# Performance work log

Measured on AMD Instinct MI355X. Metric: run time of the kernel, lower is better.

Reference implementation:

```python
import jax, jax.numpy as jnp
import numpy as np

VP = 0.4
EP = 0.21

def _c_matrix():
    # Faithfully replicate the original Ci (including its asymmetric rows 2) and invert.
    Ci = np.zeros((6, 6), dtype=np.float64)
    Ci[0, 0] = 1 / EP; Ci[0, 1] = -VP / EP; Ci[0, 2] = -VP / EP
    Ci[1, 0] = -VP / EP; Ci[1, 1] = 1 / EP; Ci[1, 2] = -VP / EP
    Ci[2, 0] = -VP;      Ci[2, 1] = -VP;      Ci[2, 2] = 1 / EP
    Ci[3, 3] = 2 * (1 + VP) / EP
    Ci[4, 4] = 2 * (1 + VP) / EP
    Ci[5, 5] = 2 * (1 + VP) / EP
    return np.linalg.inv(Ci).astype(np.float32)

C_MAT = jnp.asarray(_c_matrix())
N = 12288

def setup_inputs() -> dict:
    key = jax.random.key(0)
    k1, k2, k3 = jax.random.split(key, 3)
    xyz = jax.random.normal(k1, (N, 3), dtype=jnp.float32)
    new_xyz = jax.random.normal(k2, (N, 3), dtype=jnp.float32)
    # ~half the points are 'inside' (gt_sdf < 1e-8)
    gt_sdf = jax.random.uniform(k3, (N,), dtype=jnp.float32) - 0.5
    return {"new_xyz": new_xyz, "xyz": xyz, "gt_sdf": gt_sdf}

def reference(new_xyz, xyz, gt_sdf):
    motion = new_xyz - xyz                      # [N,3]
    inside = gt_sdf < 1e-8                      # [N] bool, selects inside points
    w = new_xyz                                 # warped coordinates (KNN space)
    n = w.shape[0]
    # Brute-force NN among inside points (KDTree k=2, second neighbor == nearest non-self).
    sq = jnp.sum(w * w, axis=1)                 # [N]
    d2 = sq[:, None] + sq[None, :] - 2.0 * (w @ w.T)   # [N,N] squared distances
    BIG = jnp.float32(1e30)
    bad_col = (~inside)[None, :] | jnp.eye(n, dtype=bool)
    d2 = jnp.where(bad_col, BIG, d2)
    nn_idx = jnp.argmin(d2, axis=1)             # nearest inside neighbor (excluding self)
    nn_d = jnp.sqrt(jnp.maximum(jnp.min(d2, axis=1), 0.0))
    # tree_list1 filter: drop rows whose nearest neighbor is a duplicate point
    valid = inside & (nn_d > 1e-8)              # [N]
    dm = motion[nn_idx] - motion                # motion_delta
    dc = w[nn_idx] - w + 1e-8                   # cords_delta (+1e-8 as in original)
    v = valid[:, None]
    dm = jnp.where(v, dm, 0.0)                  # neutralize masked rows (keep shapes static)
    dc = jnp.where(v, dc, 1.0)
    du, dv, dw = dm[:, 0], dm[:, 1], dm[:, 2]
    dx, dy, dz = dc[:, 0], dc[:, 1], dc[:, 2]
    et = jnp.stack([du / dx, dv / dy, dw / dz,
                    (du / dy + dv / dx) / 2,
                    (du / dz + dw / dx) / 2,
                    (dw / dy + dv / dz) / 2], axis=1)   # [N,6] strain tensor
    # diag(et @ C @ et.T) as an O(N) batched quadratic form
    q = jnp.einsum('ni,ij,nj->n', et, C_MAT, et)
    q = jnp.where(valid, q, 0.0)
    n_valid = jnp.sum(valid).astype(jnp.float32)
    return jnp.linalg.norm(q) / n_valid
```

## Files before the change

### kernel.cpp

```cpp
#include <hip/hip_runtime.h>
#include <math.h>
#include <string.h>

#define N 12288
#define QP 7168
#define TILE 128
#define NSPLIT 56
#define ACCS 2
#define QBLK 512
#define NQB 14
#define BT 1024

typedef unsigned long long ull;

struct CMat { float c[6][6]; };

__global__ __launch_bounds__(1024) void build_kernel(
    const float* __restrict__ new_xyz,
    const float* __restrict__ gt_sdf,
    float4* __restrict__ pts,
    int* __restrict__ cj,
    int* __restrict__ Mout)
{
    const int tid = threadIdx.x;
    const int lane = tid & 63;
    const int wave = tid >> 6;

    __shared__ int wcnt[16];
    __shared__ int sbase;
    if (tid == 0) sbase = 0;
    __syncthreads();

    for (int r = 0; r < N / BT; ++r) {
        const int idx = r * BT + tid;
        const float px = new_xyz[3 * idx + 0];
        const float py = new_xyz[3 * idx + 1];
        const float pz = new_xyz[3 * idx + 2];
        const bool ins = gt_sdf[idx] < 1e-8f;
        const ull mask = __ballot(ins);
        if (lane == 0) wcnt[wave] = __popcll(mask);
        __syncthreads();

        int pref = 0;
        for (int w = 0; w < wave; ++w) pref += wcnt[w];
        const int rank = __popcll(mask & ((1ull << lane) - 1ull));
        const int slot = sbase + pref + rank;
        if (ins && slot < QP) {
            pts[slot] = make_float4(-2.0f * px, -2.0f * py, -2.0f * pz,
                                    px * px + py * py + pz * pz);
            cj[slot] = idx;
        }
        __syncthreads();
        if (tid == 0) {
            int tot = 0;
            for (int w = 0; w < 16; ++w) tot += wcnt[w];
            sbase += tot;
        }
        __syncthreads();
    }

    const int M = sbase;
    if (tid == 0) *Mout = M;
    for (int s = M + tid; s < QP; s += BT) {
        pts[s] = make_float4(0.0f, 0.0f, 0.0f, 3e30f);
        cj[s] = 0;
    }
}

template<bool CAREFUL>
__device__ __forceinline__ void nn_inner(
    const float4* __restrict__ tile,
    const float* wx, const float* wy, const float* wz,
    const int* kx,
    float* bd, int* bk)
{
    #pragma unroll 8
    for (int k = 0; k < TILE; ++k) {
        const float4 b = tile[k];
        #pragma unroll
        for (int a = 0; a < ACCS; ++a) {
            float t = fmaf(wz[a], b.z, b.w);
            t = fmaf(wy[a], b.y, t);
            t = fmaf(wx[a], b.x, t);
            bool ok = t < bd[a];
            if (CAREFUL) ok = ok && (k != kx[a]);
            if (ok) { bd[a] = t; bk[a] = k; }
        }
    }
}

__global__ __launch_bounds__(256, 4) void nn_kernel(
    const float4* __restrict__ pts,
    ull* __restrict__ packed)
{
    const int tid = threadIdx.x;
    const int qbase = blockIdx.x * QBLK;
    const int s = blockIdx.y;
    const int jb = s * TILE;

    float wx[ACCS], wy[ACCS], wz[ACCS];
    int kx[ACCS];
    #pragma unroll
    for (int a = 0; a < ACCS; ++a) {
        const int ci = qbase + tid + a * 256;
        const float4 q = pts[ci];
        wx[a] = -0.5f * q.x;
        wy[a] = -0.5f * q.y;
        wz[a] = -0.5f * q.z;
        kx[a] = ci - jb;
    }

    __shared__ float4 tile[TILE];
    if (tid < TILE) tile[tid] = pts[jb + tid];
    __syncthreads();

    float bd[ACCS];
    int bk[ACCS];
    #pragma unroll
    for (int a = 0; a < ACCS; ++a) { bd[a] = 3.0e38f; bk[a] = 0; }

    const bool dirty = (jb < qbase + QBLK) && (jb + TILE > qbase);
    if (dirty)
        nn_inner<true>(tile, wx, wy, wz, kx, bd, bk);
    else
        nn_inner<false>(tile, wx, wy, wz, kx, bd, bk);

    #pragma unroll
    for (int a = 0; a < ACCS; ++a) {
        const int ci = qbase + tid + a * 256;
        unsigned u = __float_as_uint(bd[a]);
        u = ((int)u < 0) ? ~u : (u | 0x80000000u);
        packed[(size_t)s * QP + ci] =
            ((ull)u << 32) | (ull)(unsigned)(jb + bk[a]);
    }
}

#define NPART (QP / 256)

__global__ __launch_bounds__(256) void loss_kernel(
    const float* __restrict__ new_xyz,
    const float* __restrict__ xyz,
    const int* __restrict__ cj,
    const int* __restrict__ Mptr,
    const ull* __restrict__ packed,
    double* __restrict__ partial_sum,
    unsigned int* __restrict__ partial_cnt,
    CMat C)
{
    const int tid = threadIdx.x;
    const int ci = blockIdx.x * 256 + tid;

    ull best = ~0ull;
    #pragma unroll 8
    for (int s = 0; s < NSPLIT; ++s) {
        const ull p = packed[(size_t)s * QP + ci];
        best = (p < best) ? p : best;
    }

    const int M = *Mptr;
    const bool real = (ci < M);

    const unsigned u = (unsigned)(best >> 32);
    const unsigned bits = (u & 0x80000000u) ? (u ^ 0x80000000u) : ~u;
    const float key = __uint_as_float(bits);
    const int cc = (int)(unsigned)(best & 0xffffffffu);

    const int i  = real ? cj[ci] : 0;
    const int nn = cj[cc];

    const float wix = new_xyz[3 * i + 0];
    const float wiy = new_xyz[3 * i + 1];
    const float wiz = new_xyz[3 * i + 2];
    const float sqi = wix * wix + wiy * wiy + wiz * wiz;

    const float d2 = sqi + key;
    const float nnd = sqrtf(fmaxf(d2, 0.0f));
    const bool valid = real && (nnd > 1e-8f);

    float q = 0.0f;
    if (valid) {
        const float xix = xyz[3 * i + 0], xiy = xyz[3 * i + 1], xiz = xyz[3 * i + 2];
        const float wnx = new_xyz[3 * nn + 0], wny = new_xyz[3 * nn + 1], wnz = new_xyz[3 * nn + 2];
        const float xnx = xyz[3 * nn + 0],     xny = xyz[3 * nn + 1],     xnz = xyz[3 * nn + 2];

        const float du = (wnx - xnx) - (wix - xix);
        const float dv = (wny - xny) - (wiy - xiy);
        const float dw = (wnz - xnz) - (wiz - xiz);
        const float dx = wnx - wix + 1e-8f;
        const float dy = wny - wiy + 1e-8f;
        const float dz = wnz - wiz + 1e-8f;

        float et[6];
        et[0] = du / dx;
        et[1] = dv / dy;
        et[2] = dw / dz;
        et[3] = (du / dy + dv / dx) * 0.5f;
        et[4] = (du / dz + dw / dx) * 0.5f;
        et[5] = (dw / dy + dv / dz) * 0.5f;

        #pragma unroll
        for (int a = 0; a < 6; ++a) {
            float s2 = 0.0f;
            #pragma unroll
            for (int b2 = 0; b2 < 6; ++b2) s2 += C.c[a][b2] * et[b2];
            q += et[a] * s2;
        }
    }

    double q2 = (double)q * (double)q;
    #pragma unroll
    for (int off = 32; off > 0; off >>= 1)
        q2 += __shfl_down(q2, off, 64);
    const ull vm = __ballot(valid);
    const int lane = tid & 63;
    const int wid = tid >> 6;

    __shared__ double wsum[4];
    __shared__ unsigned wcnt2[4];
    if (lane == 0) { wsum[wid] = q2; wcnt2[wid] = (unsigned)__popcll(vm); }
    __syncthreads();
    if (tid == 0) {
        partial_sum[blockIdx.x] = wsum[0] + wsum[1] + wsum[2] + wsum[3];
        partial_cnt[blockIdx.x] = wcnt2[0] + wcnt2[1] + wcnt2[2] + wcnt2[3];
    }
}

__global__ void final_kernel(const double* __restrict__ partial_sum,
                             const unsigned int* __restrict__ partial_cnt,
                             float* __restrict__ out)
{
    const int lane = threadIdx.x;
    double s = (lane < NPART) ? partial_sum[lane] : 0.0;
    double c = (lane < NPART) ? (double)partial_cnt[lane] : 0.0;
    #pragma unroll
    for (int off = 32; off > 0; off >>= 1) {
        s += __shfl_down(s, off, 64);
        c += __shfl_down(c, off, 64);
    }
    if (lane == 0) out[0] = (float)(sqrt(s) / c);
}

static void build_cmat(CMat* M)
{
    const double VP = 0.4, EP = 0.21;
    double A[6][12];
    memset(A, 0, sizeof(A));
    double Ci[6][6];
    memset(Ci, 0, sizeof(Ci));
    Ci[0][0] = 1.0 / EP; Ci[0][1] = -VP / EP; Ci[0][2] = -VP / EP;
    Ci[1][0] = -VP / EP; Ci[1][1] = 1.0 / EP; Ci[1][2] = -VP / EP;
    Ci[2][0] = -VP;      Ci[2][1] = -VP;      Ci[2][2] = 1.0 / EP;
    Ci[3][3] = 2.0 * (1.0 + VP) / EP;
    Ci[4][4] = Ci[3][3];
    Ci[5][5] = Ci[3][3];

    for (int i = 0; i < 6; ++i) {
        for (int j = 0; j < 6; ++j) A[i][j] = Ci[i][j];
        A[i][6 + i] = 1.0;
    }
    for (int col = 0; col < 6; ++col) {
        int piv = col;
        for (int r = col + 1; r < 6; ++r)
            if (fabs(A[r][col]) > fabs(A[piv][col])) piv = r;
        if (piv != col)
            for (int c = 0; c < 12; ++c) { double t = A[col][c]; A[col][c] = A[piv][c]; A[piv][c] = t; }
        const double d = A[col][col];
        for (int c = 0; c < 12; ++c) A[col][c] /= d;
        for (int r = 0; r < 6; ++r) {
            if (r == col) continue;
            const double f = A[r][col];
            if (f == 0.0) continue;
            for (int c = 0; c < 12; ++c) A[r][c] -= f * A[col][c];
        }
    }
    for (int i = 0; i < 6; ++i)
        for (int j = 0; j < 6; ++j)
            M->c[i][j] = (float)A[i][6 + j];
}

extern "C" void kernel_launch(void* const* d_in, const int* in_sizes, int n_in,
                              void* d_out, int out_size, void* d_ws, size_t ws_size,
                              hipStream_t stream)
{
    const float* new_xyz = (const float*)d_in[0];
    const float* xyz     = (const float*)d_in[1];
    const float* gt_sdf  = (const float*)d_in[2];
    float* out = (float*)d_out;

    char* p = (char*)d_ws;
    float4* pts = (float4*)p;                    p += (size_t)QP * 16;
    int* cj = (int*)p;                           p += (size_t)QP * 4;
    int* Mptr = (int*)p;                         p += 16;
    ull* packed = (ull*)p;                       p += (size_t)NSPLIT * QP * 8;
    double* partial_sum = (double*)p;            p += NPART * sizeof(double);
    unsigned int* partial_cnt = (unsigned int*)p;

    CMat C;
    build_cmat(&C);

    build_kernel<<<1, BT, 0, stream>>>(new_xyz, gt_sdf, pts, cj, Mptr);
    nn_kernel<<<dim3(NQB, NSPLIT), 256, 0, stream>>>(pts, packed);
    loss_kernel<<<QP / 256, 256, 0, stream>>>(new_xyz, xyz, cj, Mptr, packed,
                                              partial_sum, partial_cnt, C);
    final_kernel<<<1, 64, 0, stream>>>(partial_sum, partial_cnt, out);
}
```

Measured before the change: 92.40 us.

## Merge NN partial results with atomicMin, skip empty tiles, fuse final reduction

The per-split packed nearest-neighbour candidates are no longer written to a large NSPLIT×QP buffer; each nn block now atomicMins its result into a single per-query array, so the loss kernel no longer scans 56 partials. nn blocks whose query or candidate tile lies beyond the inside-point count M exit early. The compaction kernel loads all rows up front and computes one prefix scan instead of a sync-heavy loop per round. The final reduction moves into the loss kernel through a last-block ticket, which removes one launch at the cost of 64-bit atomic contention and threadfences.

```diff
diff --git a/kernel.cpp b/kernel.cpp
--- a/kernel.cpp
+++ b/kernel.cpp
@@ -10,6 +10,8 @@
 #define QBLK 512
 #define NQB 14
 #define BT 1024
+#define RPT (N / BT)
+#define NPART (QP / 256)
 
 typedef unsigned long long ull;
 
@@ -20,51 +22,64 @@
     const float* __restrict__ gt_sdf,
     float4* __restrict__ pts,
     int* __restrict__ cj,
-    int* __restrict__ Mout)
+    int* __restrict__ Mout,
+    ull* __restrict__ best,
+    unsigned int* __restrict__ ticket)
 {
     const int tid = threadIdx.x;
     const int lane = tid & 63;
     const int wave = tid >> 6;
 
-    __shared__ int wcnt[16];
-    __shared__ int sbase;
-    if (tid == 0) sbase = 0;
-    __syncthreads();
-
-    for (int r = 0; r < N / BT; ++r) {
+    float px[RPT], py[RPT], pz[RPT];
+    unsigned flags = 0;
+
+    #pragma unroll
+    for (int r = 0; r < RPT; ++r) {
         const int idx = r * BT + tid;
-        const float px = new_xyz[3 * idx + 0];
-        const float py = new_xyz[3 * idx + 1];
-        const float pz = new_xyz[3 * idx + 2];
-        const bool ins = gt_sdf[idx] < 1e-8f;
-        const ull mask = __ballot(ins);
-        if (lane == 0) wcnt[wave] = __popcll(mask);
-        __syncthreads();
-
-        int pref = 0;
-        for (int w = 0; w < wave; ++w) pref += wcnt[w];
-        const int rank = __popcll(mask & ((1ull << lane) - 1ull));
-        const int slot = sbase + pref + rank;
-        if (ins && slot < QP) {
-            pts[slot] = make_float4(-2.0f * px, -2.0f * py, -2.0f * pz,
-                                    px * px + py * py + pz * pz);
-            cj[slot] = idx;
-        }
-        __syncthreads();
-        if (tid == 0) {
-            int tot = 0;
-            for (int w = 0; w < 16; ++w) tot += wcnt[w];
-            sbase += tot;
-        }
-        __syncthreads();
-    }
-
-    const int M = sbase;
-    if (tid == 0) *Mout = M;
+        px[r] = new_xyz[3 * idx + 0];
+        py[r] = new_xyz[3 * idx + 1];
+        pz[r] = new_xyz[3 * idx + 2];
+        if (gt_sdf[idx] < 1e-8f) flags |= (1u << r);
+    }
+
+    __shared__ int scnt[RPT * 16];
+    __shared__ int spref[RPT * 16 + 1];
+
+    #pragma unroll
+    for (int r = 0; r < RPT; ++r) {
+        const ull m = __ballot((flags >> r) & 1u);
+        if (lane == 0) scnt[r * 16 + wave] = __popcll(m);
+    }
+    __syncthreads();
+
+    if (tid < RPT * 16) {
+        int p = 0;
+        for (int f = 0; f < tid; ++f) p += scnt[f];
+        spref[tid] = p;
+        if (tid == RPT * 16 - 1) spref[RPT * 16] = p + scnt[tid];
+    }
+    __syncthreads();
+
+    const int M = spref[RPT * 16];
+
+    #pragma unroll
+    for (int r = 0; r < RPT; ++r) {
+        const ull m = __ballot((flags >> r) & 1u);
+        const int rank = __popcll(m & ((1ull << lane) - 1ull));
+        const int slot = spref[r * 16 + wave] + rank;
+        if (((flags >> r) & 1u) && slot < QP) {
+            pts[slot] = make_float4(-2.0f * px[r], -2.0f * py[r], -2.0f * pz[r],
+                                    px[r] * px[r] + py[r] * py[r] + pz[r] * pz[r]);
+            cj[slot] = r * BT + tid;
+        }
+    }
+
+    if (tid == 0) { *Mout = M; *ticket = 0u; }
     for (int s = M + tid; s < QP; s += BT) {
         pts[s] = make_float4(0.0f, 0.0f, 0.0f, 3e30f);
         cj[s] = 0;
     }
+    for (int s = tid; s < QP; s += BT) best[s] = ~0ull;
 }
 
 template<bool CAREFUL>
@@ -91,12 +106,16 @@
 
 __global__ __launch_bounds__(256, 4) void nn_kernel(
     const float4* __restrict__ pts,
-    ull* __restrict__ packed)
+    const int* __restrict__ Mptr,
+    ull* __restrict__ best)
 {
     const int tid = threadIdx.x;
     const int qbase = blockIdx.x * QBLK;
     const int s = blockIdx.y;
     const int jb = s * TILE;
+
+    const int M = *Mptr;
+    if (jb >= M || qbase >= M) return;
 
     float wx[ACCS], wy[ACCS], wz[ACCS];
     int kx[ACCS];
@@ -130,40 +149,34 @@
         const int ci = qbase + tid + a * 256;
         unsigned u = __float_as_uint(bd[a]);
         u = ((int)u < 0) ? ~u : (u | 0x80000000u);
-        packed[(size_t)s * QP + ci] =
-            ((ull)u << 32) | (ull)(unsigned)(jb + bk[a]);
-    }
-}
-
-#define NPART (QP / 256)
+        const ull v = ((ull)u << 32) | (ull)(unsigned)(jb + bk[a]);
+        atomicMin(&best[ci], v);
+    }
+}
 
 __global__ __launch_bounds__(256) void loss_kernel(
     const float* __restrict__ new_xyz,
     const float* __restrict__ xyz,
     const int* __restrict__ cj,
     const int* __restrict__ Mptr,
-    const ull* __restrict__ packed,
+    const ull* __restrict__ best_arr,
     double* __restrict__ partial_sum,
     unsigned int* __restrict__ partial_cnt,
+    unsigned int* __restrict__ ticket,
+    float* __restrict__ out,
     CMat C)
 {
     const int tid = threadIdx.x;
     const int ci = blockIdx.x * 256 + tid;
 
-    ull best = ~0ull;
-    #pragma unroll 8
-    for (int s = 0; s < NSPLIT; ++s) {
-        const ull p = packed[(size_t)s * QP + ci];
-        best = (p < best) ? p : best;
-    }
-
+    const ull best = best_arr[ci];
     const int M = *Mptr;
     const bool real = (ci < M);
 
     const unsigned u = (unsigned)(best >> 32);
     const unsigned bits = (u & 0x80000000u) ? (u ^ 0x80000000u) : ~u;
     const float key = __uint_as_float(bits);
-    const int cc = (int)(unsigned)(best & 0xffffffffu);
+    const int cc = real ? (int)(unsigned)(best & 0xffffffffu) : 0;
 
     const int i  = real ? cj[ci] : 0;
     const int nn = cj[cc];
@@ -217,27 +230,29 @@
 
     __shared__ double wsum[4];
     __shared__ unsigned wcnt2[4];
+    __shared__ bool sdone;
     if (lane == 0) { wsum[wid] = q2; wcnt2[wid] = (unsigned)__popcll(vm); }
     __syncthreads();
     if (tid == 0) {
         partial_sum[blockIdx.x] = wsum[0] + wsum[1] + wsum[2] + wsum[3];
         partial_cnt[blockIdx.x] = wcnt2[0] + wcnt2[1] + wcnt2[2] + wcnt2[3];
-    }
-}
-
-__global__ void final_kernel(const double* __restrict__ partial_sum,
-                             const unsigned int* __restrict__ partial_cnt,
-                             float* __restrict__ out)
-{
-    const int lane = threadIdx.x;
-    double s = (lane < NPART) ? partial_sum[lane] : 0.0;
-    double c = (lane < NPART) ? (double)partial_cnt[lane] : 0.0;
-    #pragma unroll
-    for (int off = 32; off > 0; off >>= 1) {
-        s += __shfl_down(s, off, 64);
-        c += __shfl_down(c, off, 64);
-    }
-    if (lane == 0) out[0] = (float)(sqrt(s) / c);
+        __threadfence();
+        const unsigned t = atomicAdd(ticket, 1u);
+        sdone = (t == NPART - 1);
+    }
+    __syncthreads();
+
+    if (sdone && tid < 64) {
+        __threadfence();
+        double s = (tid < NPART) ? partial_sum[tid] : 0.0;
+        double c = (tid < NPART) ? (double)partial_cnt[tid] : 0.0;
+        #pragma unroll
+        for (int off = 32; off > 0; off >>= 1) {
+            s += __shfl_down(s, off, 64);
+            c += __shfl_down(c, off, 64);
+        }
+        if (tid == 0) out[0] = (float)(sqrt(s) / c);
+    }
 }
 
 static void build_cmat(CMat* M)
@@ -291,16 +306,17 @@
     float4* pts = (float4*)p;                    p += (size_t)QP * 16;
     int* cj = (int*)p;                           p += (size_t)QP * 4;
     int* Mptr = (int*)p;                         p += 16;
-    ull* packed = (ull*)p;                       p += (size_t)NSPLIT * QP * 8;
+    ull* best = (ull*)p;                         p += (size_t)QP * 8;
     double* partial_sum = (double*)p;            p += NPART * sizeof(double);
-    unsigned int* partial_cnt = (unsigned int*)p;
+    unsigned int* partial_cnt = (unsigned int*)p; p += NPART * sizeof(unsigned int);
+    unsigned int* ticket = (unsigned int*)p;
 
     CMat C;
     build_cmat(&C);
 
-    build_kernel<<<1, BT, 0, stream>>>(new_xyz, gt_sdf, pts, cj, Mptr);
-    nn_kernel<<<dim3(NQB, NSPLIT), 256, 0, stream>>>(pts, packed);
-    loss_kernel<<<QP / 256, 256, 0, stream>>>(new_xyz, xyz, cj, Mptr, packed,
-                                              partial_sum, partial_cnt, C);
-    final_kernel<<<1, 64, 0, stream>>>(partial_sum, partial_cnt, out);
-}
+    build_kernel<<<1, BT, 0, stream>>>(new_xyz, gt_sdf, pts, cj, Mptr, best, ticket);
+    nn_kernel<<<dim3(NQB, NSPLIT), 256, 0, stream>>>(pts, Mptr, best);
+    loss_kernel<<<QP / 256, 256, 0, stream>>>(new_xyz, xyz, cj, Mptr, best,
+                                              partial_sum, partial_cnt, ticket,
+                                              out, C);
+}
```

Measured after the change: 80.39 us. 1.15x faster.
